# Kernel optimization log

Measured on AMD Instinct MI355X. Metric: run time of the kernel, lower is better.

Reference implementation:

```python
import jax, jax.numpy as jnp
import numpy as np

EPS = 1e-12  # torch F.normalize default eps


def setup_inputs() -> dict:
    key = jax.random.key(0)
    k1, k2, k3, k4 = jax.random.split(key, 4)
    B, M, D = 4, 8192, 512
    N, P = 128, 1
    x = jax.random.normal(k1, (B, M, D), dtype=jnp.float32)
    phi = jax.random.normal(k2, (D, N, P), dtype=jnp.float32) * (1.0 / D ** 0.5)
    scale = jnp.ones((1,), dtype=jnp.float32)
    W = jax.random.normal(k3, (N, D, D), dtype=jnp.float32) * (1.0 / D ** 0.5)
    b = jax.random.normal(k4, (N, D), dtype=jnp.float32) * 0.01
    return {"x": x, "phi": phi, "scale": scale, "W": W, "b": b}


def _l2norm(v, axis):
    return v / jnp.maximum(jnp.linalg.norm(v, axis=axis, keepdims=True), EPS)


def reference(x, phi, scale, W, b):
    # normalize tokens along feature dim, phi along dim axis, scale phi
    xn = _l2norm(x, axis=2)                      # [B,M,D]
    phin = scale * _l2norm(phi, axis=0)          # [D,N,P]
    logits = jnp.einsum('bmd,dnp->bmnp', xn, phin)
    B, M, N, P = logits.shape
    d = jax.nn.softmax(logits, axis=1)           # dispatch weights (over tokens)
    c = jax.nn.softmax(logits.reshape(B, M, N * P), axis=-1).reshape(B, M, N, P)  # combine (over slots)
    xs = jnp.einsum('bmd,bmnp->bnpd', xn, d)     # slot inputs [B,N,P,D]
    # per-expert Linear, batched over experts (grouped GEMM)
    ys = jnp.einsum('bnpd,nde->bnpe', xs, W) + b[None, :, None, :]
    y = jnp.einsum('bnpd,bmnp->bmd', ys, c)
    return y
```

## Files before the change

### kernel.cpp

```cpp
#include <hip/hip_runtime.h>
#include <math.h>

#define B_ 4
#define M_ 8192
#define D_ 512
#define N_ 128
#define TOK (B_ * M_)
#define MC_ 32
#define MLEN (M_ / MC_)

#define OFF_CS 0
#define OFF_XS (OFF_CS + 512)
#define OFF_PBT (OFF_XS + B_ * N_ * D_)
#define OFF_E (OFF_PBT + N_ * D_ / 2)
#define OFF_EWT (OFF_E + (size_t)TOK * N_)
#define OFF_XB (OFF_EWT + (size_t)N_ * TOK / 2)
#define OFF_XBT (OFF_XB + (size_t)TOK * D_ / 2)
#define OFF_YST (OFF_XBT + (size_t)D_ * TOK / 2)
#define OFF_XP (OFF_YST + B_ * D_ * N_ / 2)

typedef __attribute__((ext_vector_type(8))) short s16x8;
typedef __attribute__((ext_vector_type(4))) float f32x4;

__device__ inline short f2bf(float f) {
    union { float f; unsigned u; } v;
    v.f = f;
    unsigned r = v.u + 0x7fffu + ((v.u >> 16) & 1u);
    return (short)(r >> 16);
}

__global__ __launch_bounds__(128) void k_phinorm(const float* __restrict__ phi,
                                                 const float* __restrict__ scale,
                                                 short* __restrict__ pbt) {
    __shared__ float sred[128];
    int n = blockIdx.x, tid = threadIdx.x;
    float ss = 0.f;
    for (int d = tid; d < D_; d += 128) {
        float v = phi[d * N_ + n];
        ss += v * v;
    }
    sred[tid] = ss;
    __syncthreads();
    for (int s = 64; s > 0; s >>= 1) {
        if (tid < s) sred[tid] += sred[tid + s];
        __syncthreads();
    }
    float sc = scale[0] / fmaxf(sqrtf(sred[0]), 1e-12f);
    for (int d = tid; d < D_; d += 128) pbt[n * D_ + d] = f2bf(phi[d * N_ + n] * sc);
}

__global__ __launch_bounds__(256) void k_prep(const float* __restrict__ x,
                                              short* __restrict__ xb,
                                              short* __restrict__ xbt) {
    __shared__ short T[512 * 40];
    __shared__ float sred[32][8];
    __shared__ float srn[32];
    int t = threadIdx.x;
    int m0 = blockIdx.x * 32;
    int row = t >> 3, o8 = t & 7;
    const float4* xr = (const float4*)&x[(size_t)(m0 + row) * D_ + o8 * 64];
    float4 v[16];
    float ss = 0.f;
#pragma unroll
    for (int i = 0; i < 16; i++) {
        v[i] = xr[i];
        ss += v[i].x * v[i].x + v[i].y * v[i].y + v[i].z * v[i].z + v[i].w * v[i].w;
    }
    sred[row][o8] = ss;
    __syncthreads();
    if (t < 32) {
        float s = sred[t][0] + sred[t][1] + sred[t][2] + sred[t][3] +
                  sred[t][4] + sred[t][5] + sred[t][6] + sred[t][7];
        srn[t] = 1.0f / fmaxf(sqrtf(s), 1e-12f);
    }
    __syncthreads();
    float rv = srn[row];
    short* xrow = &xb[(size_t)(m0 + row) * D_ + o8 * 64];
    int slot = (row + 8 * (o8 & 3)) & 31;
    int dbase = o8 * 64;
#pragma unroll
    for (int i = 0; i < 16; i++) {
        short4 w = {f2bf(v[i].x * rv), f2bf(v[i].y * rv), f2bf(v[i].z * rv), f2bf(v[i].w * rv)};
        *(short4*)&xrow[i * 4] = w;
        int d = dbase + i * 4;
        T[(d + 0) * 40 + slot] = w.x;
        T[(d + 1) * 40 + slot] = w.y;
        T[(d + 2) * 40 + slot] = w.z;
        T[(d + 3) * 40 + slot] = w.w;
    }
    __syncthreads();
#pragma unroll
    for (int p = 0; p < 8; p++) {
        int d = p * 64 + (t >> 2);
        int g = t & 3;
        int sgrp = (g + ((d >> 6) & 3)) & 3;
        s16x8 val = *(const s16x8*)&T[d * 40 + sgrp * 8];
        *(s16x8*)&xbt[(size_t)d * TOK + m0 + g * 8] = val;
    }
}

__global__ __launch_bounds__(512) void k_logits(const short* __restrict__ xb,
                                                const short* __restrict__ pbt,
                                                float* __restrict__ E,
                                                short* __restrict__ ewt,
                                                float* __restrict__ colsum) {
    __shared__ short smem[2 * 128 * 40];
    short* As = smem;
    short* Bs = smem + 128 * 40;
    int t = threadIdx.x;
    int r0 = blockIdx.x * 128;
    int sm = t >> 2;
    int kq = (t & 3) * 8;
    const short* xrow = &xb[(size_t)(r0 + sm) * D_ + kq];
    const short* brow = &pbt[sm * D_ + kq];
    int wid = t >> 6, lane = t & 63;
    int quad = lane >> 4, l15 = lane & 15;
    int mw = (wid >> 1) * 32, nw = (wid & 1) * 64;
    f32x4 acc[2][4] = {};

    for (int k0 = 0; k0 < D_; k0 += 32) {
        s16x8 av = *(const s16x8*)&xrow[k0];
        s16x8 bv = *(const s16x8*)&brow[k0];
        *(s16x8*)&As[sm * 40 + kq] = av;
        *(s16x8*)&Bs[sm * 40 + kq] = bv;
        __syncthreads();
        s16x8 af[2], bf[4];
#pragma unroll
        for (int i = 0; i < 2; i++)
            af[i] = *(const s16x8*)&As[(mw + i * 16 + l15) * 40 + quad * 8];
#pragma unroll
        for (int j = 0; j < 4; j++)
            bf[j] = *(const s16x8*)&Bs[(nw + j * 16 + l15) * 40 + quad * 8];
#pragma unroll
        for (int i = 0; i < 2; i++)
#pragma unroll
            for (int j = 0; j < 4; j++)
                acc[i][j] = __builtin_amdgcn_mfma_f32_16x16x32_bf16(af[i], bf[j], acc[i][j], 0, 0, 0);
        __syncthreads();
    }
    int bb = r0 >> 13;
    short4 ebf[2][4];
#pragma unroll
    for (int j = 0; j < 4; j++) {
        int n = nw + j * 16 + l15;
        float cs = 0.f;
#pragma unroll
        for (int i = 0; i < 2; i++) {
            int mb = r0 + mw + i * 16 + quad * 4;
            f32x4 vv = acc[i][j];
            float e0 = __expf(vv[0]), e1 = __expf(vv[1]), e2 = __expf(vv[2]), e3 = __expf(vv[3]);
            cs += e0 + e1 + e2 + e3;
            E[(size_t)(mb + 0) * N_ + n] = e0;
            E[(size_t)(mb + 1) * N_ + n] = e1;
            E[(size_t)(mb + 2) * N_ + n] = e2;
            E[(size_t)(mb + 3) * N_ + n] = e3;
            short4 eb = {f2bf(e0), f2bf(e1), f2bf(e2), f2bf(e3)};
            ebf[i][j] = eb;
        }
        cs += __shfl_xor(cs, 16, 64);
        cs += __shfl_xor(cs, 32, 64);
        if (lane < 16) atomicAdd(&colsum[bb * N_ + n], cs);
    }
    short* T = smem;
#pragma unroll
    for (int h = 0; h < 2; h++) {
        if ((wid & 1) == h) {
#pragma unroll
            for (int i = 0; i < 2; i++) {
                int mb = mw + i * 16 + quad * 4;
#pragma unroll
                for (int j = 0; j < 4; j++) {
                    int nl = j * 16 + l15;
                    *(short4*)&T[nl * 136 + mb] = ebf[i][j];
                }
            }
        }
        __syncthreads();
        {
            int nl = t >> 3, c = t & 7;
            s16x8 v0 = *(const s16x8*)&T[nl * 136 + c * 16];
            s16x8 v1 = *(const s16x8*)&T[nl * 136 + c * 16 + 8];
            size_t go = (size_t)(h * 64 + nl) * TOK + r0 + c * 16;
            *(s16x8*)&ewt[go] = v0;
            *(s16x8*)&ewt[go + 8] = v1;
        }
        __syncthreads();
    }
}

__global__ __launch_bounds__(256) void k_xs(const short* __restrict__ ewt,
                                            const short* __restrict__ xbt,
                                            float* __restrict__ part) {
    __shared__ short An[128 * 40];
    __shared__ short Bd[128 * 40];
    int t = threadIdx.x, bi = blockIdx.x;
    int dt = bi & 3, mc = (bi >> 2) & 31, b = bi >> 7;
    int d0 = dt * 128;
    size_t mbase = (size_t)b * M_ + (size_t)mc * MLEN;
    int srow = t >> 1, shalf = (t & 1) * 16;
    const short* arow = &ewt[(size_t)srow * TOK + mbase + shalf];
    const short* brow = &xbt[(size_t)(d0 + srow) * TOK + mbase + shalf];
    int wid = t >> 6, lane = t & 63;
    int quad = lane >> 4, l15 = lane & 15;
    int nw = (wid >> 1) * 64, dw = (wid & 1) * 64;
    f32x4 acc[4][4] = {};

    for (int k0 = 0; k0 < MLEN; k0 += 32) {
        s16x8 a0 = *(const s16x8*)&arow[k0];
        s16x8 a1 = *(const s16x8*)&arow[k0 + 8];
        s16x8 b0 = *(const s16x8*)&brow[k0];
        s16x8 b1 = *(const s16x8*)&brow[k0 + 8];
        *(s16x8*)&An[srow * 40 + shalf] = a0;
        *(s16x8*)&An[srow * 40 + shalf + 8] = a1;
        *(s16x8*)&Bd[srow * 40 + shalf] = b0;
        *(s16x8*)&Bd[srow * 40 + shalf + 8] = b1;
        __syncthreads();
        s16x8 af[4], bf[4];
#pragma unroll
        for (int i = 0; i < 4; i++)
            af[i] = *(const s16x8*)&An[(nw + i * 16 + l15) * 40 + quad * 8];
#pragma unroll
        for (int j = 0; j < 4; j++)
            bf[j] = *(const s16x8*)&Bd[(dw + j * 16 + l15) * 40 + quad * 8];
#pragma unroll
        for (int i = 0; i < 4; i++)
#pragma unroll
            for (int j = 0; j < 4; j++)
                acc[i][j] = __builtin_amdgcn_mfma_f32_16x16x32_bf16(af[i], bf[j], acc[i][j], 0, 0, 0);
        __syncthreads();
    }
    size_t pbase = (((size_t)mc * B_ + b) * N_) * D_ + d0;
#pragma unroll
    for (int i = 0; i < 4; i++) {
        int nb = nw + i * 16 + quad * 4;
#pragma unroll
        for (int j = 0; j < 4; j++) {
            int d = dw + j * 16 + l15;
            f32x4 vv = acc[i][j];
            part[pbase + (size_t)(nb + 0) * D_ + d] = vv[0];
            part[pbase + (size_t)(nb + 1) * D_ + d] = vv[1];
            part[pbase + (size_t)(nb + 2) * D_ + d] = vv[2];
            part[pbase + (size_t)(nb + 3) * D_ + d] = vv[3];
        }
    }
}

__global__ __launch_bounds__(256) void k_xsum(const float* __restrict__ part,
                                              const float* __restrict__ colsum,
                                              float* __restrict__ xs) {
    int bi = blockIdx.x;
    int tid = threadIdx.x;
    float inv = 1.0f / colsum[bi];
    size_t base = (size_t)bi * D_ + tid * 2;
    float sx = 0.f, sy = 0.f;
#pragma unroll 8
    for (int mc = 0; mc < MC_; mc++) {
        float2 v = *(const float2*)&part[(size_t)mc * (B_ * N_ * D_) + base];
        sx += v.x;
        sy += v.y;
    }
    float2 o = {sx * inv, sy * inv};
    *(float2*)&xs[base] = o;
}

__global__ __launch_bounds__(256) void k_ys(const float* __restrict__ xs,
                                            const float* __restrict__ W,
                                            const float* __restrict__ bias,
                                            short* __restrict__ ysT) {
    __shared__ float xsn[B_][D_];
    int bi = blockIdx.x;
    int n = bi >> 2, eq = bi & 3;
    int tid = threadIdx.x;
    {
        int lb = tid >> 6, ld = (tid & 63) * 4;
        *(float4*)&xsn[lb][ld] = *(const float4*)&xs[((size_t)lb * N_ + n) * D_ + ld];
        *(float4*)&xsn[lb][256 + ld] =
            *(const float4*)&xs[((size_t)lb * N_ + n) * D_ + 256 + ld];
    }
    __syncthreads();
    int b = tid >> 6;
    int e = eq * 128 + (tid & 63) * 2;
    const float* Wn = W + (size_t)n * D_ * D_ + e;
    float a0 = 0.f, a1 = 0.f;
#pragma unroll 8
    for (int d = 0; d < D_; d++) {
        float2 w = *(const float2*)&Wn[(size_t)d * D_];
        float xv = xsn[b][d];
        a0 += xv * w.x;
        a1 += xv * w.y;
    }
    float2 bv = *(const float2*)&bias[n * D_ + e];
    ysT[((size_t)b * D_ + e) * N_ + n] = f2bf(a0 + bv.x);
    ysT[((size_t)b * D_ + e + 1) * N_ + n] = f2bf(a1 + bv.y);
}

__global__ __launch_bounds__(256) void k_combine(const float* __restrict__ E,
                                                 const short* __restrict__ ysT,
                                                 float* __restrict__ y) {
    __shared__ short As[128 * 40];
    __shared__ short Bs[128 * 40];
    __shared__ float rsA[2][128];
    __shared__ float rsinv[128];
    int t = threadIdx.x, bi = blockIdx.x;
    int dt = bi & 3, mt = bi >> 2;
    int r0 = mt * 128, d0 = dt * 128;
    int bb = r0 >> 13;
    int sm = t >> 1, nh = (t & 1) * 16;
    const float* erow = &E[(size_t)(r0 + sm) * N_ + nh];
    const short* yrow = &ysT[((size_t)bb * D_ + d0 + sm) * N_ + nh];
    int wid = t >> 6, lane = t & 63;
    int quad = lane >> 4, l15 = lane & 15;
    int mw = (wid >> 1) * 64, dw = (wid & 1) * 64;
    f32x4 acc[4][4] = {};
    float rsp = 0.f;

    for (int ks = 0; ks < 4; ks++) {
        int n0 = ks * 32;
        float4 e0 = *(const float4*)&erow[n0];
        float4 e1 = *(const float4*)&erow[n0 + 4];
        float4 e2 = *(const float4*)&erow[n0 + 8];
        float4 e3 = *(const float4*)&erow[n0 + 12];
        rsp += e0.x + e0.y + e0.z + e0.w + e1.x + e1.y + e1.z + e1.w +
               e2.x + e2.y + e2.z + e2.w + e3.x + e3.y + e3.z + e3.w;
        short4 w0 = {f2bf(e0.x), f2bf(e0.y), f2bf(e0.z), f2bf(e0.w)};
        short4 w1 = {f2bf(e1.x), f2bf(e1.y), f2bf(e1.z), f2bf(e1.w)};
        short4 w2 = {f2bf(e2.x), f2bf(e2.y), f2bf(e2.z), f2bf(e2.w)};
        short4 w3 = {f2bf(e3.x), f2bf(e3.y), f2bf(e3.z), f2bf(e3.w)};
        *(short4*)&As[sm * 40 + nh + 0] = w0;
        *(short4*)&As[sm * 40 + nh + 4] = w1;
        *(short4*)&As[sm * 40 + nh + 8] = w2;
        *(short4*)&As[sm * 40 + nh + 12] = w3;
        *(s16x8*)&Bs[sm * 40 + nh] = *(const s16x8*)&yrow[n0];
        *(s16x8*)&Bs[sm * 40 + nh + 8] = *(const s16x8*)&yrow[n0 + 8];
        __syncthreads();
        s16x8 af[4], bf[4];
#pragma unroll
        for (int i = 0; i < 4; i++)
            af[i] = *(const s16x8*)&As[(mw + i * 16 + l15) * 40 + quad * 8];
#pragma unroll
        for (int j = 0; j < 4; j++)
            bf[j] = *(const s16x8*)&Bs[(dw + j * 16 + l15) * 40 + quad * 8];
#pragma unroll
        for (int i = 0; i < 4; i++)
#pragma unroll
            for (int j = 0; j < 4; j++)
                acc[i][j] = __builtin_amdgcn_mfma_f32_16x16x32_bf16(af[i], bf[j], acc[i][j], 0, 0, 0);
        __syncthreads();
    }
    rsA[t & 1][sm] = rsp;
    __syncthreads();
    if (t < 128) rsinv[t] = 1.0f / (rsA[0][t] + rsA[1][t]);
    __syncthreads();
#pragma unroll
    for (int i = 0; i < 4; i++) {
        int mb = mw + i * 16 + quad * 4;
        float i0 = rsinv[mb], i1 = rsinv[mb + 1], i2 = rsinv[mb + 2], i3 = rsinv[mb + 3];
#pragma unroll
        for (int j = 0; j < 4; j++) {
            int d = d0 + dw + j * 16 + l15;
            f32x4 v = acc[i][j];
            y[(size_t)(r0 + mb + 0) * D_ + d] = v[0] * i0;
            y[(size_t)(r0 + mb + 1) * D_ + d] = v[1] * i1;
            y[(size_t)(r0 + mb + 2) * D_ + d] = v[2] * i2;
            y[(size_t)(r0 + mb + 3) * D_ + d] = v[3] * i3;
        }
    }
}

extern "C" void kernel_launch(void* const* d_in, const int* in_sizes, int n_in,
                              void* d_out, int out_size, void* d_ws, size_t ws_size,
                              hipStream_t stream) {
    const float* x = (const float*)d_in[0];
    const float* phi = (const float*)d_in[1];
    const float* scale = (const float*)d_in[2];
    const float* W = (const float*)d_in[3];
    const float* bias = (const float*)d_in[4];
    float* y = (float*)d_out;
    float* ws = (float*)d_ws;

    float* colsum = ws + OFF_CS;
    float* xs = ws + OFF_XS;
    short* pbt = (short*)(ws + OFF_PBT);
    float* E = ws + OFF_E;
    short* ewt = (short*)(ws + OFF_EWT);
    short* xb = (short*)(ws + OFF_XB);
    short* xbt = (short*)(ws + OFF_XBT);
    short* ysT = (short*)(ws + OFF_YST);
    float* part = ws + OFF_XP;

    hipMemsetAsync(colsum, 0, 512 * sizeof(float), stream);

    k_phinorm<<<N_, 128, 0, stream>>>(phi, scale, pbt);
    k_prep<<<TOK / 32, 256, 0, stream>>>(x, xb, xbt);
    k_logits<<<TOK / 128, 512, 0, stream>>>(xb, pbt, E, ewt, colsum);
    k_xs<<<B_ * MC_ * 4, 256, 0, stream>>>(ewt, xbt, part);
    k_xsum<<<B_ * N_, 256, 0, stream>>>(part, colsum, xs);
    k_ys<<<N_ * 4, 256, 0, stream>>>(xs, W, bias, ysT);
    k_combine<<<(TOK / 128) * 4, 256, 0, stream>>>(E, ysT, y);
}
```

Measured before the change: 355.5 us.

## Fuse token normalization and transpose into logits GEMM; swizzle block order

Removes the separate prep kernel. The logits kernel now reads fp32 x directly, converts it to bf16 on the fly, and accumulates the row sum of squares. It applies the inverse norm to the logits after the GEMM, and writes the transposed bf16 x as a side output. Because the transposed x is now unnormalized, the per-token inverse norm is folded into the bf16 dispatch weights so the slot-input GEMM still yields normalized inputs. The goal is to drop the intermediate xb buffer write and read and one launch. The change also halves the M-chunk count for k_xs and adds a block-index swizzle to k_xs and k_combine, intended to improve cache locality.

```diff
diff --git a/kernel.cpp b/kernel.cpp
--- a/kernel.cpp
+++ b/kernel.cpp
@@ -6,7 +6,7 @@
 #define D_ 512
 #define N_ 128
 #define TOK (B_ * M_)
-#define MC_ 32
+#define MC_ 16
 #define MLEN (M_ / MC_)
 
 #define OFF_CS 0
@@ -14,8 +14,7 @@
 #define OFF_PBT (OFF_XS + B_ * N_ * D_)
 #define OFF_E (OFF_PBT + N_ * D_ / 2)
 #define OFF_EWT (OFF_E + (size_t)TOK * N_)
-#define OFF_XB (OFF_EWT + (size_t)N_ * TOK / 2)
-#define OFF_XBT (OFF_XB + (size_t)TOK * D_ / 2)
+#define OFF_XBT (OFF_EWT + (size_t)N_ * TOK / 2)
 #define OFF_YST (OFF_XBT + (size_t)D_ * TOK / 2)
 #define OFF_XP (OFF_YST + B_ * D_ * N_ / 2)
 
@@ -49,77 +48,37 @@
     for (int d = tid; d < D_; d += 128) pbt[n * D_ + d] = f2bf(phi[d * N_ + n] * sc);
 }
 
-__global__ __launch_bounds__(256) void k_prep(const float* __restrict__ x,
-                                              short* __restrict__ xb,
-                                              short* __restrict__ xbt) {
-    __shared__ short T[512 * 40];
-    __shared__ float sred[32][8];
-    __shared__ float srn[32];
-    int t = threadIdx.x;
-    int m0 = blockIdx.x * 32;
-    int row = t >> 3, o8 = t & 7;
-    const float4* xr = (const float4*)&x[(size_t)(m0 + row) * D_ + o8 * 64];
-    float4 v[16];
-    float ss = 0.f;
-#pragma unroll
-    for (int i = 0; i < 16; i++) {
-        v[i] = xr[i];
-        ss += v[i].x * v[i].x + v[i].y * v[i].y + v[i].z * v[i].z + v[i].w * v[i].w;
-    }
-    sred[row][o8] = ss;
-    __syncthreads();
-    if (t < 32) {
-        float s = sred[t][0] + sred[t][1] + sred[t][2] + sred[t][3] +
-                  sred[t][4] + sred[t][5] + sred[t][6] + sred[t][7];
-        srn[t] = 1.0f / fmaxf(sqrtf(s), 1e-12f);
-    }
-    __syncthreads();
-    float rv = srn[row];
-    short* xrow = &xb[(size_t)(m0 + row) * D_ + o8 * 64];
-    int slot = (row + 8 * (o8 & 3)) & 31;
-    int dbase = o8 * 64;
-#pragma unroll
-    for (int i = 0; i < 16; i++) {
-        short4 w = {f2bf(v[i].x * rv), f2bf(v[i].y * rv), f2bf(v[i].z * rv), f2bf(v[i].w * rv)};
-        *(short4*)&xrow[i * 4] = w;
-        int d = dbase + i * 4;
-        T[(d + 0) * 40 + slot] = w.x;
-        T[(d + 1) * 40 + slot] = w.y;
-        T[(d + 2) * 40 + slot] = w.z;
-        T[(d + 3) * 40 + slot] = w.w;
-    }
-    __syncthreads();
-#pragma unroll
-    for (int p = 0; p < 8; p++) {
-        int d = p * 64 + (t >> 2);
-        int g = t & 3;
-        int sgrp = (g + ((d >> 6) & 3)) & 3;
-        s16x8 val = *(const s16x8*)&T[d * 40 + sgrp * 8];
-        *(s16x8*)&xbt[(size_t)d * TOK + m0 + g * 8] = val;
-    }
-}
-
-__global__ __launch_bounds__(512) void k_logits(const short* __restrict__ xb,
+__global__ __launch_bounds__(512) void k_logits(const float* __restrict__ x,
                                                 const short* __restrict__ pbt,
                                                 float* __restrict__ E,
                                                 short* __restrict__ ewt,
+                                                short* __restrict__ xbt,
                                                 float* __restrict__ colsum) {
     __shared__ short smem[2 * 128 * 40];
+    __shared__ float rnS[128];
     short* As = smem;
     short* Bs = smem + 128 * 40;
     int t = threadIdx.x;
     int r0 = blockIdx.x * 128;
     int sm = t >> 2;
     int kq = (t & 3) * 8;
-    const short* xrow = &xb[(size_t)(r0 + sm) * D_ + kq];
+    const float* xrow = &x[(size_t)(r0 + sm) * D_ + kq];
     const short* brow = &pbt[sm * D_ + kq];
     int wid = t >> 6, lane = t & 63;
     int quad = lane >> 4, l15 = lane & 15;
     int mw = (wid >> 1) * 32, nw = (wid & 1) * 64;
+    int dl = t & 31, mg = t >> 5;
     f32x4 acc[2][4] = {};
+    float ss = 0.f;
 
     for (int k0 = 0; k0 < D_; k0 += 32) {
-        s16x8 av = *(const s16x8*)&xrow[k0];
+        float4 a0 = *(const float4*)&xrow[k0];
+        float4 a1 = *(const float4*)&xrow[k0 + 4];
+        ss += a0.x * a0.x + a0.y * a0.y + a0.z * a0.z + a0.w * a0.w +
+              a1.x * a1.x + a1.y * a1.y + a1.z * a1.z + a1.w * a1.w;
+        s16x8 av;
+        av[0] = f2bf(a0.x); av[1] = f2bf(a0.y); av[2] = f2bf(a0.z); av[3] = f2bf(a0.w);
+        av[4] = f2bf(a1.x); av[5] = f2bf(a1.y); av[6] = f2bf(a1.z); av[7] = f2bf(a1.w);
         s16x8 bv = *(const s16x8*)&brow[k0];
         *(s16x8*)&As[sm * 40 + kq] = av;
         *(s16x8*)&Bs[sm * 40 + kq] = bv;
@@ -136,9 +95,27 @@
 #pragma unroll
             for (int j = 0; j < 4; j++)
                 acc[i][j] = __builtin_amdgcn_mfma_f32_16x16x32_bf16(af[i], bf[j], acc[i][j], 0, 0, 0);
-        __syncthreads();
-    }
+        {
+            s16x8 tv;
+#pragma unroll
+            for (int r = 0; r < 8; r++) tv[r] = As[(mg * 8 + r) * 40 + dl];
+            *(s16x8*)&xbt[(size_t)(k0 + dl) * TOK + r0 + mg * 8] = tv;
+        }
+        __syncthreads();
+    }
+    ss += __shfl_xor(ss, 1, 64);
+    ss += __shfl_xor(ss, 2, 64);
+    if ((t & 3) == 0) rnS[sm] = 1.0f / fmaxf(sqrtf(ss), 1e-12f);
+    __syncthreads();
+
     int bb = r0 >> 13;
+    float rv[2][4];
+#pragma unroll
+    for (int i = 0; i < 2; i++) {
+        int ml = mw + i * 16 + quad * 4;
+        rv[i][0] = rnS[ml]; rv[i][1] = rnS[ml + 1];
+        rv[i][2] = rnS[ml + 2]; rv[i][3] = rnS[ml + 3];
+    }
     short4 ebf[2][4];
 #pragma unroll
     for (int j = 0; j < 4; j++) {
@@ -148,13 +125,15 @@
         for (int i = 0; i < 2; i++) {
             int mb = r0 + mw + i * 16 + quad * 4;
             f32x4 vv = acc[i][j];
-            float e0 = __expf(vv[0]), e1 = __expf(vv[1]), e2 = __expf(vv[2]), e3 = __expf(vv[3]);
+            float e0 = __expf(vv[0] * rv[i][0]), e1 = __expf(vv[1] * rv[i][1]);
+            float e2 = __expf(vv[2] * rv[i][2]), e3 = __expf(vv[3] * rv[i][3]);
             cs += e0 + e1 + e2 + e3;
             E[(size_t)(mb + 0) * N_ + n] = e0;
             E[(size_t)(mb + 1) * N_ + n] = e1;
             E[(size_t)(mb + 2) * N_ + n] = e2;
             E[(size_t)(mb + 3) * N_ + n] = e3;
-            short4 eb = {f2bf(e0), f2bf(e1), f2bf(e2), f2bf(e3)};
+            short4 eb = {f2bf(e0 * rv[i][0]), f2bf(e1 * rv[i][1]),
+                         f2bf(e2 * rv[i][2]), f2bf(e3 * rv[i][3])};
             ebf[i][j] = eb;
         }
         cs += __shfl_xor(cs, 16, 64);
@@ -193,8 +172,10 @@
                                             float* __restrict__ part) {
     __shared__ short An[128 * 40];
     __shared__ short Bd[128 * 40];
-    int t = threadIdx.x, bi = blockIdx.x;
-    int dt = bi & 3, mc = (bi >> 2) & 31, b = bi >> 7;
+    int t = threadIdx.x;
+    int bid = blockIdx.x;
+    int bi = (bid & 7) * 32 + (bid >> 3);
+    int dt = bi & 3, mc = (bi >> 2) & 15, b = bi >> 6;
     int d0 = dt * 128;
     size_t mbase = (size_t)b * M_ + (size_t)mc * MLEN;
     int srow = t >> 1, shalf = (t & 1) * 16;
@@ -301,7 +282,9 @@
     __shared__ short Bs[128 * 40];
     __shared__ float rsA[2][128];
     __shared__ float rsinv[128];
-    int t = threadIdx.x, bi = blockIdx.x;
+    int t = threadIdx.x;
+    int bid = blockIdx.x;
+    int bi = (bid & 7) * 128 + (bid >> 3);
     int dt = bi & 3, mt = bi >> 2;
     int r0 = mt * 128, d0 = dt * 128;
     int bb = r0 >> 13;
@@ -383,7 +366,6 @@
     short* pbt = (short*)(ws + OFF_PBT);
     float* E = ws + OFF_E;
     short* ewt = (short*)(ws + OFF_EWT);
-    short* xb = (short*)(ws + OFF_XB);
     short* xbt = (short*)(ws + OFF_XBT);
     short* ysT = (short*)(ws + OFF_YST);
     float* part = ws + OFF_XP;
@@ -391,8 +373,7 @@
     hipMemsetAsync(colsum, 0, 512 * sizeof(float), stream);
 
     k_phinorm<<<N_, 128, 0, stream>>>(phi, scale, pbt);
-    k_prep<<<TOK / 32, 256, 0, stream>>>(x, xb, xbt);
-    k_logits<<<TOK / 128, 512, 0, stream>>>(xb, pbt, E, ewt, colsum);
+    k_logits<<<TOK / 128, 512, 0, stream>>>(x, pbt, E, ewt, xbt, colsum);
     k_xs<<<B_ * MC_ * 4, 256, 0, stream>>>(ewt, xbt, part);
     k_xsum<<<B_ * N_, 256, 0, stream>>>(part, colsum, xs);
     k_ys<<<N_ * 4, 256, 0, stream>>>(xs, W, bias, ysT);
```

Result: faster. 327.1 us (-8.0%).
